# Performance work log

Hardware: AMD Instinct MI355X
Metric: run time of the kernel (lower is better)

## Reference

```python
import jax, jax.numpy as jnp
import numpy as np

B, S, D_MODEL, D_K, D_V, N_HEAD = 2, 2048, 1024, 1024, 1024, 16


def setup_inputs() -> dict:
    key = jax.random.key(0)
    k1, k2, k3, k4, k5, k6, k7 = jax.random.split(key, 7)
    s = 1.0 / np.sqrt(D_MODEL)
    return {
        "q": jax.random.normal(k1, (B, S, D_MODEL), dtype=jnp.float32),
        "k": jax.random.normal(k2, (B, S, D_MODEL), dtype=jnp.float32),
        "v": jax.random.normal(k3, (B, S, D_MODEL), dtype=jnp.float32),
        "Wq": jax.random.normal(k4, (D_MODEL, D_K), dtype=jnp.float32) * s,
        "Wk": jax.random.normal(k5, (D_MODEL, D_K), dtype=jnp.float32) * s,
        "Wv": jax.random.normal(k6, (D_MODEL, D_V), dtype=jnp.float32) * s,
        "Wp": jax.random.normal(k7, (D_V, D_MODEL), dtype=jnp.float32) * (1.0 / np.sqrt(D_V)),
    }


def reference(q, k, v, Wq, Wk, Wv, Wp):
    b, sq, _ = q.shape
    sk = k.shape[1]
    hd_k = D_K // N_HEAD
    hd_v = D_V // N_HEAD
    # Faithful to original: plain row-major reshape (B,S,d) -> (B,H,S,d/H),
    # i.e. the sequence axis is split across heads (as torch .view does here).
    Q = (q @ Wq).reshape(b, N_HEAD, sq, hd_k)
    K = (k @ Wk).reshape(b, N_HEAD, sk, hd_k)
    V = (v @ Wv).reshape(b, N_HEAD, sk, hd_v)
    # No 1/sqrt(d_k) scaling in the original module.
    wei = jnp.einsum('bhqd,bhkd->bhqk', Q, K)
    # causal mask (masked=True): tril(ones(sq, sk))
    causal = jnp.arange(sq)[:, None] >= jnp.arange(sk)[None, :]
    wei = jnp.where(causal[None, None], wei, -jnp.inf)
    att = jnp.einsum('bhqk,bhkd->bhqd', jax.nn.softmax(wei, axis=-1), V)
    out = jnp.swapaxes(att, 1, 2).reshape(b, sq, D_V)
    return out @ Wp
```

## Files before the change

### kernel.cpp

```cpp
#include <hip/hip_runtime.h>
#include <cstdint>
#include <cstddef>


typedef _Float16 f16;
typedef _Float16 f16x8 __attribute__((ext_vector_type(8)));
typedef float f32x4 __attribute__((ext_vector_type(4)));

#define NB 2
#define NS 2048
#define NDM 1024
#define NHEAD 16

__device__ __forceinline__ void gload16(void* lds, const void* g) {
    __builtin_amdgcn_global_load_lds(
        (__attribute__((address_space(1))) void*)g,
        (__attribute__((address_space(3))) void*)lds, 16, 0, 0);
}

__device__ __forceinline__ float fast_exp2(float x) {
#if __has_builtin(__builtin_amdgcn_exp2f)
    return __builtin_amdgcn_exp2f(x);
#else
    return __expf(x * 0.69314718055994531f);
#endif
}

__global__ __launch_bounds__(256) void prep_kernel(
    const float* __restrict__ q, const float* __restrict__ k, const float* __restrict__ v,
    f16* __restrict__ qb, f16* __restrict__ kb, f16* __restrict__ vb,
    const float* __restrict__ w0, const float* __restrict__ w1,
    const float* __restrict__ w2, const float* __restrict__ w3,
    f16* __restrict__ t0, f16* __restrict__ t1, f16* __restrict__ t2, f16* __restrict__ t3)
{
    __shared__ float tile[32][33];
    const int bx = blockIdx.x, tid = threadIdx.x;
    if (bx < 6144) {
        const int arr = bx >> 11;
        const float* s = arr == 0 ? q : (arr == 1 ? k : v);
        f16* d        = arr == 0 ? qb : (arr == 1 ? kb : vb);
        int vi = (bx & 2047) * 256 + tid;
        const float4* sp = (const float4*)s;
        float4 a = sp[vi * 2 + 0];
        float4 b = sp[vi * 2 + 1];
        f16x8 h;
        h[0] = (f16)a.x; h[1] = (f16)a.y; h[2] = (f16)a.z; h[3] = (f16)a.w;
        h[4] = (f16)b.x; h[5] = (f16)b.y; h[6] = (f16)b.z; h[7] = (f16)b.w;
        *(f16x8*)(d + (size_t)vi * 8) = h;
    } else {
        const int t = bx - 6144;
        const int mat = t >> 10, tl = t & 1023;
        const float* W; f16* T;
        switch (mat) {
            case 0: W = w0; T = t0; break;
            case 1: W = w1; T = t1; break;
            case 2: W = w2; T = t2; break;
            default: W = w3; T = t3; break;
        }
        const int n = 1024;
        const int tx = tid & 31, ty = tid >> 5;
        const int c0 = (tl & 31) * 32, r0 = (tl >> 5) * 32;
        #pragma unroll
        for (int i = 0; i < 32; i += 8)
            tile[ty + i][tx] = W[(size_t)(r0 + ty + i) * n + c0 + tx];
        __syncthreads();
        #pragma unroll
        for (int i = 0; i < 32; i += 8)
            T[(size_t)(c0 + ty + i) * n + r0 + tx] = (f16)tile[tx][ty + i];
    }
}

template <typename CT>
__device__ __forceinline__ void gemm_abt_body(
    const f16* __restrict__ A, const f16* __restrict__ Bt, CT* __restrict__ C,
    int M, int N, int K, int bx, int by, float cscale)
{
    __shared__ f16 As[128][64];
    __shared__ f16 Bs[128][64];
    const int tid  = threadIdx.x;
    const int lane = tid & 63, wave = tid >> 6;
    const int quad = lane >> 4, ln = lane & 15;
    const int wm = wave >> 1, wn = wave & 1;
    const int m0 = by * 128, n0 = bx * 128;
    const int r8 = lane >> 3, c8 = lane & 7;
    const int swz = ((c8 ^ r8) * 8);

    f32x4 acc[4][4] = {};
    for (int k0 = 0; k0 < K; k0 += 64) {
        __syncthreads();
        #pragma unroll
        for (int i = 0; i < 4; i++) {
            int blk = wave * 4 + i;
            int row = blk * 8 + r8;
            gload16(&As[blk * 8][0], &A [(size_t)(m0 + row) * K + k0 + swz]);
            gload16(&Bs[blk * 8][0], &Bt[(size_t)(n0 + row) * K + k0 + swz]);
        }
        __syncthreads();
        #pragma unroll
        for (int kc = 0; kc < 2; kc++) {
            f16x8 af[4], bfr[4];
            #pragma unroll
            for (int mt = 0; mt < 4; mt++)
                af[mt] = *(const f16x8*)&As[wm * 64 + mt * 16 + ln][((kc * 4 + quad) ^ (ln & 7)) * 8];
            #pragma unroll
            for (int nt = 0; nt < 4; nt++)
                bfr[nt] = *(const f16x8*)&Bs[wn * 64 + nt * 16 + ln][((kc * 4 + quad) ^ (ln & 7)) * 8];
            #pragma unroll
            for (int mt = 0; mt < 4; mt++)
                #pragma unroll
                for (int nt = 0; nt < 4; nt++)
                    acc[mt][nt] = __builtin_amdgcn_mfma_f32_16x16x32_f16(af[mt], bfr[nt], acc[mt][nt], 0, 0, 0);
        }
    }
    #pragma unroll
    for (int mt = 0; mt < 4; mt++)
        #pragma unroll
        for (int nt = 0; nt < 4; nt++)
            #pragma unroll
            for (int r = 0; r < 4; r++) {
                int row = m0 + wm * 64 + mt * 16 + quad * 4 + r;
                int col = n0 + wn * 64 + nt * 16 + ln;
                C[(size_t)row * N + col] = (CT)(acc[mt][nt][r] * cscale);
            }
}

__global__ __launch_bounds__(256) void gemm3_kernel(
    const f16* __restrict__ a0, const f16* __restrict__ a1, const f16* __restrict__ a2,
    const f16* __restrict__ b0, const f16* __restrict__ b1, const f16* __restrict__ b2,
    f16* __restrict__ c0, f16* __restrict__ c1, f16* __restrict__ c2, int M, int N, int K)
{
    const f16 *A, *Bt; f16* C; float sc;
    switch (blockIdx.z) {
        case 0: A = a0; Bt = b0; C = c0; sc = 1.4426950408889634f; break;
        case 1: A = a1; Bt = b1; C = c1; sc = 1.0f; break;
        default: A = a2; Bt = b2; C = c2; sc = 1.0f; break;
    }
    gemm_abt_body<f16>(A, Bt, C, M, N, K, blockIdx.x, blockIdx.y, sc);
}

__global__ __launch_bounds__(256) void gemm_out_kernel(
    const f16* __restrict__ A, const f16* __restrict__ Bt, float* __restrict__ C,
    int M, int N, int K)
{
    __shared__ f16 As[128][64];
    __shared__ f16 Bs[64][64];
    const int tid  = threadIdx.x;
    const int lane = tid & 63, wave = tid >> 6;
    const int quad = lane >> 4, ln = lane & 15;
    const int m0 = blockIdx.y * 128, n0 = blockIdx.x * 64;
    const int r8 = lane >> 3, c8 = lane & 7;
    const int swz = ((c8 ^ r8) * 8);

    f32x4 acc[2][4] = {};
    for (int k0 = 0; k0 < K; k0 += 64) {
        __syncthreads();
        #pragma unroll
        for (int i = 0; i < 4; i++) {
            int blk = wave * 4 + i;
            gload16(&As[blk * 8][0], &A[(size_t)(m0 + blk * 8 + r8) * K + k0 + swz]);
        }
        #pragma unroll
        for (int i = 0; i < 2; i++) {
            int blk = wave * 2 + i;
            gload16(&Bs[blk * 8][0], &Bt[(size_t)(n0 + blk * 8 + r8) * K + k0 + swz]);
        }
        __syncthreads();
        #pragma unroll
        for (int kc = 0; kc < 2; kc++) {
            f16x8 af[2], bfr[4];
            #pragma unroll
            for (int mt = 0; mt < 2; mt++)
                af[mt] = *(const f16x8*)&As[wave * 32 + mt * 16 + ln][((kc * 4 + quad) ^ (ln & 7)) * 8];
            #pragma unroll
            for (int nt = 0; nt < 4; nt++)
                bfr[nt] = *(const f16x8*)&Bs[nt * 16 + ln][((kc * 4 + quad) ^ (ln & 7)) * 8];
            #pragma unroll
            for (int mt = 0; mt < 2; mt++)
                #pragma unroll
                for (int nt = 0; nt < 4; nt++)
                    acc[mt][nt] = __builtin_amdgcn_mfma_f32_16x16x32_f16(af[mt], bfr[nt], acc[mt][nt], 0, 0, 0);
        }
    }
    #pragma unroll
    for (int mt = 0; mt < 2; mt++)
        #pragma unroll
        for (int nt = 0; nt < 4; nt++)
            #pragma unroll
            for (int r = 0; r < 4; r++) {
                int row = m0 + wave * 32 + mt * 16 + quad * 4 + r;
                int col = n0 + nt * 16 + ln;
                C[(size_t)row * N + col] = acc[mt][nt][r];
            }
}

__global__ __launch_bounds__(256) void vtrans_kernel(
    const f16* __restrict__ Vp, f16* __restrict__ Vt)
{
    const int kt = blockIdx.x;
    const int h  = blockIdx.y;
    const int b  = blockIdx.z;
    const f16* src = Vp + (size_t)b * (NS * NDM) + (size_t)h * (128 * NDM);
    f16* dst = Vt + (size_t)(b * NHEAD + h) * (64 * 2048);

    __shared__ f16 Ls[64][64];
    const int tid = threadIdx.x;
    #pragma unroll
    for (int i = 0; i < 2; i++) {
        int vi = tid + i * 256;
        int key = vi >> 3, c = vi & 7;
        int cs = c ^ ((key >> 3) & 7);
        *(uint4*)&Ls[key][cs * 8] = *(const uint4*)&src[(size_t)(kt * 64 + key) * 64 + c * 8];
    }
    __syncthreads();
    #pragma unroll
    for (int i = 0; i < 2; i++) {
        int vi = tid + i * 256;
        int d2 = vi >> 3, kc = vi & 7;
        int cs = (d2 >> 3) ^ kc;
        f16 tmp[8];
        #pragma unroll
        for (int j = 0; j < 8; j++)
            tmp[j] = Ls[kc * 8 + j][cs * 8 + (d2 & 7)];
        *(uint4*)&dst[(size_t)d2 * 2048 + kt * 64 + kc * 8] = *(uint4*)tmp;
    }
}

__global__ __launch_bounds__(256) void attn_kernel(
    const f16* __restrict__ Qp, const f16* __restrict__ Kp, const f16* __restrict__ Vt,
    f16* __restrict__ att)
{
    const int p = blockIdx.x;
    const int h = blockIdx.y;
    const int b = blockIdx.z;
    const size_t hb = (size_t)b * (NS * NDM) + (size_t)h * (128 * NDM);
    const f16* Qh = Qp + hb;
    const f16* Kh = Kp + hb;
    const f16* Vh = Vt + (size_t)(b * NHEAD + h) * (64 * 2048);

    __shared__ f16 PQ[64][136];
    __shared__ f16 Ks[128][64];
    __shared__ f16 Vs[64][128];

    const int tid  = threadIdx.x;
    const int lane = tid & 63, wave = tid >> 6;
    const int quad = lane >> 4, ln = lane & 15;
    const int r8 = lane >> 3, c8 = lane & 7;
    const int r4 = lane >> 4, c16 = lane & 15;

    f16x8 ones;
    #pragma unroll
    for (int j = 0; j < 8; j++) ones[j] = (f16)1.0f;

    for (int pass = 0; pass < 2; pass++) {
        const int qt = pass == 0 ? (31 - p) : p;
        __syncthreads();
        #pragma unroll
        for (int i = 0; i < 2; i++) {
            int vi = tid + i * 256;
            int row = vi >> 3, kk = (vi & 7) * 8;
            *(uint4*)&PQ[row][kk] = *(const uint4*)&Qh[(size_t)(qt * 64 + row) * 64 + kk];
        }
        __syncthreads();
        f16x8 qf[2];
        #pragma unroll
        for (int kc = 0; kc < 2; kc++)
            qf[kc] = *(const f16x8*)&PQ[wave * 16 + ln][kc * 32 + quad * 8];

        float m_i[4];
        #pragma unroll
        for (int r = 0; r < 4; r++) m_i[r] = -3e30f;
        f32x4 o[4] = {};
        f32x4 o5 = {};

        const int nkt = (qt + 2) >> 1;
        for (int kt = 0; kt < nkt; kt++) {
            __syncthreads();
            #pragma unroll
            for (int i = 0; i < 4; i++) {
                int blk = wave * 4 + i;
                int krow = blk * 8 + r8;
                gload16(&Ks[blk * 8][0], &Kh[(size_t)(kt * 128 + krow) * 64 + ((c8 ^ r8) * 8)]);
                int vrow = blk * 4 + r4;
                gload16(&Vs[blk * 4][0], &Vh[(size_t)vrow * 2048 + kt * 128 + ((c16 ^ (vrow & 15)) * 8)]);
            }
            __syncthreads();

            f32x4 sf[8] = {};
            #pragma unroll
            for (int kc = 0; kc < 2; kc++)
                #pragma unroll
                for (int ct = 0; ct < 8; ct++) {
                    int krow = ct * 16 + ln;
                    f16x8 kf = *(const f16x8*)&Ks[krow][((kc * 4 + quad) ^ (ln & 7)) * 8];
                    sf[ct] = __builtin_amdgcn_mfma_f32_16x16x32_f16(qf[kc], kf, sf[ct], 0, 0, 0);
                }

            if (kt == nkt - 1) {
                #pragma unroll
                for (int ct = 0; ct < 8; ct++) {
                    int jg = kt * 128 + ct * 16 + ln;
                    #pragma unroll
                    for (int r = 0; r < 4; r++) {
                        int ig = qt * 64 + wave * 16 + quad * 4 + r;
                        if (jg > ig) sf[ct][r] = -3e30f;
                    }
                }
            }

            #pragma unroll
            for (int r = 0; r < 4; r++) {
                float tm = sf[0][r];
                #pragma unroll
                for (int ct = 1; ct < 8; ct++) tm = fmaxf(tm, sf[ct][r]);
                #pragma unroll
                for (int off = 1; off < 16; off <<= 1) tm = fmaxf(tm, __shfl_xor(tm, off, 64));
                float mnew = fmaxf(m_i[r], tm);
                float a = fast_exp2(m_i[r] - mnew);
                m_i[r] = mnew;
                #pragma unroll
                for (int ct = 0; ct < 8; ct++)
                    sf[ct][r] = fast_exp2(sf[ct][r] - mnew);
                #pragma unroll
                for (int vt = 0; vt < 4; vt++) o[vt][r] *= a;
                o5[r] *= a;
            }

            #pragma unroll
            for (int ct = 0; ct < 8; ct++)
                #pragma unroll
                for (int r = 0; r < 4; r++)
                    PQ[wave * 16 + quad * 4 + r][ct * 16 + ln] = (f16)sf[ct][r];

            #pragma unroll
            for (int kc = 0; kc < 4; kc++) {
                f16x8 pa = *(const f16x8*)&PQ[wave * 16 + ln][kc * 32 + quad * 8];
                #pragma unroll
                for (int vt = 0; vt < 4; vt++) {
                    int vrow = vt * 16 + ln;
                    f16x8 vb = *(const f16x8*)&Vs[vrow][(((kc * 4 + quad) ^ ln) & 15) * 8];
                    o[vt] = __builtin_amdgcn_mfma_f32_16x16x32_f16(pa, vb, o[vt], 0, 0, 0);
                }
                o5 = __builtin_amdgcn_mfma_f32_16x16x32_f16(pa, ones, o5, 0, 0, 0);
            }
        }

        #pragma unroll
        for (int r = 0; r < 4; r++) {
            float inv = 1.0f / o5[r];
            int s2 = qt * 64 + wave * 16 + quad * 4 + r;
            #pragma unroll
            for (int vt = 0; vt < 4; vt++) {
                int d2 = vt * 16 + ln;
                att[((size_t)b * NS + s2) * NDM + h * 64 + d2] = (f16)(o[vt][r] * inv);
            }
        }
    }
}

extern "C" void kernel_launch(void* const* d_in, const int* in_sizes, int n_in,
                              void* d_out, int out_size, void* d_ws, size_t ws_size,
                              hipStream_t stream)
{
    const float* q  = (const float*)d_in[0];
    const float* k  = (const float*)d_in[1];
    const float* v  = (const float*)d_in[2];
    const float* Wq = (const float*)d_in[3];
    const float* Wk = (const float*)d_in[4];
    const float* Wv = (const float*)d_in[5];
    const float* Wp = (const float*)d_in[6];
    float* out = (float*)d_out;

    char* ws = (char*)d_ws;
    const size_t MB = 1024 * 1024;
    f16* qb   = (f16*)(ws + 0 * MB);
    f16* kb   = (f16*)(ws + 8 * MB);
    f16* vb   = (f16*)(ws + 16 * MB);
    f16* Wqt  = (f16*)(ws + 24 * MB);
    f16* Wkt  = (f16*)(ws + 26 * MB);
    f16* Wvt  = (f16*)(ws + 28 * MB);
    f16* Wpt  = (f16*)(ws + 30 * MB);
    f16* Qp   = (f16*)(ws + 32 * MB);
    f16* Kp   = (f16*)(ws + 40 * MB);
    f16* Vp   = (f16*)(ws + 48 * MB);
    f16* attb = (f16*)(ws + 56 * MB);
    f16* Vtg  = vb;

    const int M = NB * NS;
    const int N = NDM;
    const int K = NDM;

    prep_kernel<<<dim3(10240), 256, 0, stream>>>(q, k, v, qb, kb, vb,
                                                 Wq, Wk, Wv, Wp, Wqt, Wkt, Wvt, Wpt);
    gemm3_kernel<<<dim3(N / 128, M / 128, 3), 256, 0, stream>>>(qb, kb, vb, Wqt, Wkt, Wvt, Qp, Kp, Vp, M, N, K);
    vtrans_kernel<<<dim3(32, NHEAD, NB), 256, 0, stream>>>(Vp, Vtg);
    attn_kernel<<<dim3(16, NHEAD, NB), 256, 0, stream>>>(Qp, Kp, Vtg, attb);
    gemm_out_kernel<<<dim3(N / 64, M / 128), 256, 0, stream>>>(attb, Wpt, out, M, N, K);
}
```

Before: 239.7 us.

## Remap block indices to group tiles by XCD for L2 locality

Launches all four kernels on a flat 1D grid and decodes block coordinates so that consecutive block IDs (round-robin across the 8 XCDs) map to tiles sharing the same A rows, heads, or batch on each XCD. The aim is to improve L2 reuse of shared operand tiles in the GEMMs and attention, and to spread work evenly across dies. The remaining loop-variable renames only avoid name clashes. The remapping relies on fixed problem sizes and on the hardware's round-robin dispatch order.

```diff
diff --git a/kernel.cpp b/kernel.cpp
--- a/kernel.cpp
+++ b/kernel.cpp
@@ -129,25 +129,41 @@
     const f16* __restrict__ b0, const f16* __restrict__ b1, const f16* __restrict__ b2,
     f16* __restrict__ c0, f16* __restrict__ c1, f16* __restrict__ c2, int M, int N, int K)
 {
+    const int f = blockIdx.x;
+    const int t = f & 7;
+    const int r = f >> 3;
+    const int idx = r & 3;
+    const int r2 = r >> 2;
+    const int bx = r2 & 7;
+    const int z = r2 >> 3;
+    const int by = 16 * (t & 1) + ((t >> 1) & 3) + 4 * idx;
+
     const f16 *A, *Bt; f16* C; float sc;
-    switch (blockIdx.z) {
+    switch (z) {
         case 0: A = a0; Bt = b0; C = c0; sc = 1.4426950408889634f; break;
         case 1: A = a1; Bt = b1; C = c1; sc = 1.0f; break;
         default: A = a2; Bt = b2; C = c2; sc = 1.0f; break;
     }
-    gemm_abt_body<f16>(A, Bt, C, M, N, K, blockIdx.x, blockIdx.y, sc);
+    gemm_abt_body<f16>(A, Bt, C, M, N, K, bx, by, sc);
 }
 
 __global__ __launch_bounds__(256) void gemm_out_kernel(
     const f16* __restrict__ A, const f16* __restrict__ Bt, float* __restrict__ C,
     int M, int N, int K)
 {
+    const int f = blockIdx.x;
+    const int a7 = f & 7;
+    const int r = f >> 3;
+    const int idx = r & 3;
+    const int bx = r >> 2;
+    const int by = a7 + 8 * idx;
+
     __shared__ f16 As[128][64];
     __shared__ f16 Bs[64][64];
     const int tid  = threadIdx.x;
     const int lane = tid & 63, wave = tid >> 6;
     const int quad = lane >> 4, ln = lane & 15;
-    const int m0 = blockIdx.y * 128, n0 = blockIdx.x * 64;
+    const int m0 = by * 128, n0 = bx * 64;
     const int r8 = lane >> 3, c8 = lane & 7;
     const int swz = ((c8 ^ r8) * 8);
 
@@ -186,19 +202,24 @@
         #pragma unroll
         for (int nt = 0; nt < 4; nt++)
             #pragma unroll
-            for (int r = 0; r < 4; r++) {
-                int row = m0 + wave * 32 + mt * 16 + quad * 4 + r;
+            for (int r4 = 0; r4 < 4; r4++) {
+                int row = m0 + wave * 32 + mt * 16 + quad * 4 + r4;
                 int col = n0 + nt * 16 + ln;
-                C[(size_t)row * N + col] = acc[mt][nt][r];
+                C[(size_t)row * N + col] = acc[mt][nt][r4];
             }
 }
 
 __global__ __launch_bounds__(256) void vtrans_kernel(
     const f16* __restrict__ Vp, f16* __restrict__ Vt)
 {
-    const int kt = blockIdx.x;
-    const int h  = blockIdx.y;
-    const int b  = blockIdx.z;
+    const int f = blockIdx.x;
+    const int t = f & 7;
+    const int r = f >> 3;
+    const int kt = r & 31;
+    const int idxh = r >> 5;
+    const int b = t & 1;
+    const int h = ((t >> 1) & 3) + 4 * idxh;
+
     const f16* src = Vp + (size_t)b * (NS * NDM) + (size_t)h * (128 * NDM);
     f16* dst = Vt + (size_t)(b * NHEAD + h) * (64 * 2048);
 
@@ -229,9 +250,14 @@
     const f16* __restrict__ Qp, const f16* __restrict__ Kp, const f16* __restrict__ Vt,
     f16* __restrict__ att)
 {
-    const int p = blockIdx.x;
-    const int h = blockIdx.y;
-    const int b = blockIdx.z;
+    const int f = blockIdx.x;
+    const int t = f & 7;
+    const int r = f >> 3;
+    const int p = r & 15;
+    const int idxh = r >> 4;
+    const int b = t & 1;
+    const int h = ((t >> 1) & 3) + 4 * idxh;
+
     const size_t hb = (size_t)b * (NS * NDM) + (size_t)h * (128 * NDM);
     const f16* Qh = Qp + hb;
     const f16* Kh = Kp + hb;
@@ -268,7 +294,7 @@
 
         float m_i[4];
         #pragma unroll
-        for (int r = 0; r < 4; r++) m_i[r] = -3e30f;
+        for (int r2 = 0; r2 < 4; r2++) m_i[r2] = -3e30f;
         f32x4 o[4] = {};
         f32x4 o5 = {};
 
@@ -300,36 +326,36 @@
                 for (int ct = 0; ct < 8; ct++) {
                     int jg = kt * 128 + ct * 16 + ln;
                     #pragma unroll
-                    for (int r = 0; r < 4; r++) {
-                        int ig = qt * 64 + wave * 16 + quad * 4 + r;
-                        if (jg > ig) sf[ct][r] = -3e30f;
+                    for (int r2 = 0; r2 < 4; r2++) {
+                        int ig = qt * 64 + wave * 16 + quad * 4 + r2;
+                        if (jg > ig) sf[ct][r2] = -3e30f;
                     }
                 }
             }
 
             #pragma unroll
-            for (int r = 0; r < 4; r++) {
-                float tm = sf[0][r];
-                #pragma unroll
-                for (int ct = 1; ct < 8; ct++) tm = fmaxf(tm, sf[ct][r]);
+            for (int r2 = 0; r2 < 4; r2++) {
+                float tm = sf[0][r2];
+                #pragma unroll
+                for (int ct = 1; ct < 8; ct++) tm = fmaxf(tm, sf[ct][r2]);
                 #pragma unroll
                 for (int off = 1; off < 16; off <<= 1) tm = fmaxf(tm, __shfl_xor(tm, off, 64));
-                float mnew = fmaxf(m_i[r], tm);
-                float a = fast_exp2(m_i[r] - mnew);
-                m_i[r] = mnew;
+                float mnew = fmaxf(m_i[r2], tm);
+                float a = fast_exp2(m_i[r2] - mnew);
+                m_i[r2] = mnew;
                 #pragma unroll
                 for (int ct = 0; ct < 8; ct++)
-                    sf[ct][r] = fast_exp2(sf[ct][r] - mnew);
-                #pragma unroll
-                for (int vt = 0; vt < 4; vt++) o[vt][r] *= a;
-                o5[r] *= a;
+                    sf[ct][r2] = fast_exp2(sf[ct][r2] - mnew);
+                #pragma unroll
+                for (int vt = 0; vt < 4; vt++) o[vt][r2] *= a;
+                o5[r2] *= a;
             }
 
             #pragma unroll
             for (int ct = 0; ct < 8; ct++)
                 #pragma unroll
-                for (int r = 0; r < 4; r++)
-                    PQ[wave * 16 + quad * 4 + r][ct * 16 + ln] = (f16)sf[ct][r];
+                for (int r2 = 0; r2 < 4; r2++)
+                    PQ[wave * 16 + quad * 4 + r2][ct * 16 + ln] = (f16)sf[ct][r2];
 
             #pragma unroll
             for (int kc = 0; kc < 4; kc++) {
@@ -345,13 +371,13 @@
         }
 
         #pragma unroll
-        for (int r = 0; r < 4; r++) {
-            float inv = 1.0f / o5[r];
-            int s2 = qt * 64 + wave * 16 + quad * 4 + r;
+        for (int r2 = 0; r2 < 4; r2++) {
+            float inv = 1.0f / o5[r2];
+            int s2 = qt * 64 + wave * 16 + quad * 4 + r2;
             #pragma unroll
             for (int vt = 0; vt < 4; vt++) {
                 int d2 = vt * 16 + ln;
-                att[((size_t)b * NS + s2) * NDM + h * 64 + d2] = (f16)(o[vt][r] * inv);
+                att[((size_t)b * NS + s2) * NDM + h * 64 + d2] = (f16)(o[vt][r2] * inv);
             }
         }
     }
@@ -391,8 +417,8 @@
 
     prep_kernel<<<dim3(10240), 256, 0, stream>>>(q, k, v, qb, kb, vb,
                                                  Wq, Wk, Wv, Wp, Wqt, Wkt, Wvt, Wpt);
-    gemm3_kernel<<<dim3(N / 128, M / 128, 3), 256, 0, stream>>>(qb, kb, vb, Wqt, Wkt, Wvt, Qp, Kp, Vp, M, N, K);
-    vtrans_kernel<<<dim3(32, NHEAD, NB), 256, 0, stream>>>(Vp, Vtg);
-    attn_kernel<<<dim3(16, NHEAD, NB), 256, 0, stream>>>(Qp, Kp, Vtg, attb);
-    gemm_out_kernel<<<dim3(N / 64, M / 128), 256, 0, stream>>>(attb, Wpt, out, M, N, K);
-}
+    gemm3_kernel<<<dim3(768), 256, 0, stream>>>(qb, kb, vb, Wqt, Wkt, Wvt, Qp, Kp, Vp, M, N, K);
+    vtrans_kernel<<<dim3(1024), 256, 0, stream>>>(Vp, Vtg);
+    attn_kernel<<<dim3(512), 256, 0, stream>>>(Qp, Kp, Vtg, attb);
+    gemm_out_kernel<<<dim3(512), 256, 0, stream>>>(attb, Wpt, out, M, N, K);
+}
```

Result: faster. 214.1 us (-10.7%).
